# Kernel optimization log

Measured on AMD Instinct MI355X. Metric: run time of the kernel, lower is better.

## Reference

```python
import jax, jax.numpy as jnp
import numpy as np

D = 128          # node_state_dim
N_NODES = 5000
WINDOW = 10
N_TOTAL = WINDOW * N_NODES
E = 131072       # structural (int) edges
T = 2            # message passing steps
HID = 1024


def setup_inputs() -> dict:
    key = jax.random.key(0)
    ks = jax.random.split(key, 20)
    ie = jax.random.randint(ks[0], (E, 3), 0, N_NODES, dtype=jnp.int32)
    int_edges = jnp.stack([ie[:, 0] % WINDOW, ie[:, 1], ie[:, 2]], axis=1)
    nodes = jax.random.randint(ks[1], (N_NODES,), 0, 10, dtype=jnp.int32)

    def init(k, shape, scale=0.05):
        return (jax.random.normal(k, shape, jnp.float32) * scale)

    params = dict(
        embed_table=init(ks[2], (10, D)),
        msg_W1=init(ks[3], (2 * D, HID)), msg_b1=jnp.zeros((HID,), jnp.float32),
        msg_W2=init(ks[4], (HID, D)), msg_b2=jnp.zeros((D,), jnp.float32),
        gru_int_W=init(ks[5], (D, 3 * D)), gru_int_U=init(ks[6], (D, 3 * D)),
        gru_int_b=jnp.zeros((2, 3 * D), jnp.float32),
        gru_temp_W=init(ks[7], (D, 3 * D)), gru_temp_U=init(ks[8], (D, 3 * D)),
        gru_temp_b=jnp.zeros((2, 3 * D), jnp.float32),
        ro_W1=init(ks[9], (D, HID)), ro_b1=jnp.zeros((HID,), jnp.float32),
        ro_W2=init(ks[10], (HID, 512)), ro_b2=jnp.zeros((512,), jnp.float32),
        ro_W3=init(ks[11], (512, 10)), ro_b3=jnp.zeros((10,), jnp.float32),
    )
    return {"int_edges": int_edges, "nodes": nodes, **params}


def _temp_edges():
    fwd_src = np.arange(0, N_TOTAL - N_NODES)
    fwd_dst = fwd_src + N_NODES
    bwd_src = np.arange(N_NODES, N_TOTAL)
    bwd_dst = bwd_src - N_NODES
    src = jnp.asarray(np.concatenate([fwd_src, bwd_src]), jnp.int32)
    dst = jnp.asarray(np.concatenate([fwd_dst, bwd_dst]), jnp.int32)
    return src, dst


def _gru(x, h, W, U, b):
    # Keras GRUCell, reset_after=True. x,h: [N,D]; W,U: [D,3D]; b: [2,3D]
    xg = x @ W + b[0]
    hg = h @ U + b[1]
    xz, xr, xh = jnp.split(xg, 3, axis=-1)
    hz, hr, hh = jnp.split(hg, 3, axis=-1)
    z = jax.nn.sigmoid(xz + hz)
    r = jax.nn.sigmoid(xr + hr)
    hcand = jnp.tanh(xh + r * hh)
    return z * h + (1.0 - z) * hcand


def _msg(x, W1, b1, W2, b2):
    # Dense(1024,relu) -> Dropout(inference: identity) -> Dense(D,relu)
    return jax.nn.relu(jax.nn.relu(x @ W1 + b1) @ W2 + b2)


def _seg_mean(x, idx, n):
    s = jax.ops.segment_sum(x, idx, num_segments=n)
    c = jax.ops.segment_sum(jnp.ones((x.shape[0],), x.dtype), idx, num_segments=n)
    return jnp.where(c[:, None] > 0, s / jnp.maximum(c, 1.0)[:, None], 0.0)


def reference(int_edges, nodes, embed_table, msg_W1, msg_b1, msg_W2, msg_b2,
              gru_int_W, gru_int_U, gru_int_b, gru_temp_W, gru_temp_U, gru_temp_b,
              ro_W1, ro_b1, ro_W2, ro_b2, ro_W3, ro_b3):
    node_idx = int_edges[:, 0] * N_NODES + int_edges[:, 1]        # [E]
    neigh_idx = int_edges[:, 0] * N_NODES + int_edges[:, 2]       # [E]
    t_src, t_dst = _temp_edges()

    h = embed_table[nodes]                                        # [n_nodes, D]
    h = jnp.repeat(h, WINDOW, axis=0)                             # [N_TOTAL, D]

    for _ in range(T):
        # structural edges
        m_in = jnp.concatenate([h[node_idx], h[neigh_idx]], axis=1)   # [E, 2D]
        m = _msg(m_in, msg_W1, msg_b1, msg_W2, msg_b2)                # [E, D]
        agg = _seg_mean(m, neigh_idx, N_TOTAL)                        # [N_TOTAL, D]
        h = _gru(agg, h, gru_int_W, gru_int_U, gru_int_b)
        # temporal edges
        tm_in = jnp.concatenate([h[t_src], h[t_dst]], axis=1)
        tm = _msg(tm_in, msg_W1, msg_b1, msg_W2, msg_b2)
        tagg = _seg_mean(tm, t_dst, N_TOTAL)
        h = _gru(tagg, h, gru_temp_W, gru_temp_U, gru_temp_b)

    # readout on first frame's nodes
    x = h[:N_NODES]
    x = jax.nn.relu(x @ ro_W1 + ro_b1)
    x = jax.nn.relu(x @ ro_W2 + ro_b2)
    return jax.nn.softmax(x @ ro_W3 + ro_b3, axis=-1)
```

## Files before the change

### kernel.cpp

```cpp
#include <hip/hip_runtime.h>
#include <math.h>

#define D 128
#define N_NODES 5000
#define WINDOW 10
#define N_TOTAL 50000
#define NE_INT 131072
#define NE_TMP 90000
#define NE_FWD (N_TOTAL - N_NODES)
#define HID 1024

typedef short bf16x8 __attribute__((ext_vector_type(8)));
typedef float f32x4 __attribute__((ext_vector_type(4)));

#define SA 264
#define SH 136
#define SK 136
#define SCAN_B 256

static __device__ __forceinline__ short f2bf(float f) {
    union { float f; unsigned u; } v; v.f = f;
    unsigned r = v.u + 0x7fffu + ((v.u >> 16) & 1u);
    return (short)(r >> 16);
}
static __device__ __forceinline__ float bf2f(short s) {
    union { unsigned u; float f; } v;
    v.u = ((unsigned)(unsigned short)s) << 16;
    return v.f;
}
static __device__ __forceinline__ float lo_bf(unsigned u) {
    union { unsigned u; float f; } v; v.u = u << 16; return v.f;
}
static __device__ __forceinline__ float hi_bf(unsigned u) {
    union { unsigned u; float f; } v; v.u = u & 0xffff0000u; return v.f;
}

__global__ void k_tcvt(const float* __restrict__ in, short* __restrict__ out, int K, int N) {
    int i = blockIdx.x * blockDim.x + threadIdx.x;
    if (i >= N * K) return;
    int n = i / K, k = i - n * K;
    out[i] = f2bf(in[(size_t)k * N + n]);
}

__global__ void k_init_h(const int* __restrict__ nodes, const float* __restrict__ embed,
                         float* __restrict__ h32, short* __restrict__ h16) {
    int i = blockIdx.x * blockDim.x + threadIdx.x;
    if (i >= N_TOTAL * D) return;
    int row = i >> 7;
    int c = i & 127;
    int n = nodes[row / WINDOW];
    float v = embed[n * D + c];
    h32[i] = v;
    h16[i] = f2bf(v);
}

__global__ void k_build_int_edges(const int* __restrict__ ie, int* __restrict__ src,
                                  int* __restrict__ dst, int* __restrict__ icnt) {
    int e = blockIdx.x * blockDim.x + threadIdx.x;
    if (e >= NE_INT) return;
    int t = ie[e * 3 + 0], a = ie[e * 3 + 1], b = ie[e * 3 + 2];
    int d = t * N_NODES + b;
    src[e] = t * N_NODES + a;
    dst[e] = d;
    atomicAdd(&icnt[d], 1);
}

__global__ void k_build_tmp_edges(int* __restrict__ src, int* __restrict__ dst) {
    int e = blockIdx.x * blockDim.x + threadIdx.x;
    if (e >= NE_TMP) return;
    int s, d;
    if (e < NE_FWD) { s = e; d = e + N_NODES; }
    else { int q = e - NE_FWD; s = q + N_NODES; d = q; }
    src[e] = s;
    dst[e] = d;
}

__global__ void k_scan_partial(const int* __restrict__ cnt, int* __restrict__ rowstart,
                               int* __restrict__ btot, int n) {
    __shared__ int s[SCAN_B];
    int tid = threadIdx.x;
    int i = blockIdx.x * SCAN_B + tid;
    int v = (i < n) ? cnt[i] : 0;
    s[tid] = v;
    __syncthreads();
    for (int off = 1; off < SCAN_B; off <<= 1) {
        int x = (tid >= off) ? s[tid - off] : 0;
        __syncthreads();
        s[tid] += x;
        __syncthreads();
    }
    if (i < n) rowstart[i] = s[tid] - v;
    if (tid == SCAN_B - 1) btot[blockIdx.x] = s[tid];
}

__global__ void k_scan_block(int* __restrict__ btot, int nb) {
    __shared__ int s[SCAN_B];
    int tid = threadIdx.x;
    int v = (tid < nb) ? btot[tid] : 0;
    s[tid] = v;
    __syncthreads();
    for (int off = 1; off < SCAN_B; off <<= 1) {
        int x = (tid >= off) ? s[tid - off] : 0;
        __syncthreads();
        s[tid] += x;
        __syncthreads();
    }
    if (tid < nb) btot[tid] = s[tid] - v;
}

__global__ void k_scan_add(int* __restrict__ rowstart, const int* __restrict__ btot,
                           int* __restrict__ cursor, int n, int total) {
    int i = blockIdx.x * blockDim.x + threadIdx.x;
    if (i < n) {
        int v = rowstart[i] + btot[i >> 8];
        rowstart[i] = v;
        cursor[i] = v;
    }
    if (i == 0) rowstart[n] = total;
}

__global__ void k_fill_csr(const int* __restrict__ dst, int nE, int* __restrict__ cursor,
                           int* __restrict__ pmap) {
    int e = blockIdx.x * blockDim.x + threadIdx.x;
    if (e >= nE) return;
    int p = atomicAdd(&cursor[dst[e]], 1);
    pmap[e] = p;
}

__global__ void __launch_bounds__(256, 2) k_msg_mfma(
    const short* __restrict__ h16, const int* __restrict__ src, const int* __restrict__ dst,
    const int* __restrict__ pmap, int nE,
    const short* __restrict__ W1T, const float* __restrict__ b1,
    const short* __restrict__ W2T, const float* __restrict__ b2,
    short* __restrict__ m)
{
    __shared__ short Ain[64 * SA];
    __shared__ short Hid[64 * SH];

    int t = threadIdx.x;
    int e0 = blockIdx.x * 64;

    {
        int r = t >> 2, q = t & 3;
        int e = e0 + r;
        int ec = (e < nE) ? e : (nE - 1);
        int s = src[ec], d = dst[ec];
        const uint4* ps = (const uint4*)(h16 + (size_t)s * D);
        const uint4* pd = (const uint4*)(h16 + (size_t)d * D);
        uint4* ao = (uint4*)(Ain + r * SA);
#pragma unroll
        for (int i = 0; i < 8; ++i) {
            int g = i * 4 + q;
            ao[g] = (i < 4) ? ps[g] : pd[g - 16];
        }
    }
    __syncthreads();

    int w = t >> 6, lane = t & 63;
    int lm = lane & 15, lk = lane >> 4;

    f32x4 c2[2][4];
#pragma unroll
    for (int cs = 0; cs < 2; ++cs) {
        int out0 = w * 32 + cs * 16 + lk * 4;
#pragma unroll
        for (int et = 0; et < 4; ++et)
#pragma unroll
            for (int rg = 0; rg < 4; ++rg) c2[cs][et][rg] = b2[out0 + rg];
    }

    f32x4 c1[2][4];
#pragma unroll
    for (int cs = 0; cs < 2; ++cs) {
        int ch0 = (2 * w + cs) * 16 + lk * 4;
#pragma unroll
        for (int et = 0; et < 4; ++et)
#pragma unroll
            for (int rg = 0; rg < 4; ++rg) c1[cs][et][rg] = b1[ch0 + rg];
    }
#pragma unroll
    for (int kk = 0; kk < 8; ++kk) {
        int ko = kk * 32 + lk * 8;
        bf16x8 a0 = *(const bf16x8*)(W1T + (size_t)((2 * w) * 16 + lm) * 256 + ko);
        bf16x8 a1 = *(const bf16x8*)(W1T + (size_t)((2 * w + 1) * 16 + lm) * 256 + ko);
        bf16x8 bf[4];
#pragma unroll
        for (int et = 0; et < 4; ++et)
            bf[et] = *(const bf16x8*)(Ain + (et * 16 + lm) * SA + ko);
#pragma unroll
        for (int et = 0; et < 4; ++et) {
            c1[0][et] = __builtin_amdgcn_mfma_f32_16x16x32_bf16(a0, bf[et], c1[0][et], 0, 0, 0);
            c1[1][et] = __builtin_amdgcn_mfma_f32_16x16x32_bf16(a1, bf[et], c1[1][et], 0, 0, 0);
        }
    }

    for (int hc = 0; hc < 8; ++hc) {
        __syncthreads();
#pragma unroll
        for (int cs = 0; cs < 2; ++cs) {
            int ch_in = (2 * w + cs) * 16 + lk * 4;
#pragma unroll
            for (int et = 0; et < 4; ++et) {
                int edge = et * 16 + lm;
                short4 sv;
                sv.x = f2bf(fmaxf(c1[cs][et][0], 0.f));
                sv.y = f2bf(fmaxf(c1[cs][et][1], 0.f));
                sv.z = f2bf(fmaxf(c1[cs][et][2], 0.f));
                sv.w = f2bf(fmaxf(c1[cs][et][3], 0.f));
                *(short4*)(Hid + edge * SH + ch_in) = sv;
            }
        }
        __syncthreads();

        if (hc < 7) {
#pragma unroll
            for (int cs = 0; cs < 2; ++cs) {
                int ch0 = (hc + 1) * 128 + (2 * w + cs) * 16 + lk * 4;
#pragma unroll
                for (int et = 0; et < 4; ++et)
#pragma unroll
                    for (int rg = 0; rg < 4; ++rg) c1[cs][et][rg] = b1[ch0 + rg];
            }
        }
#pragma unroll
        for (int kk = 0; kk < 8; ++kk) {
            int ko = kk * 32 + lk * 8;
            if (kk < 4) {
                bf16x8 a0 = *(const bf16x8*)(W2T + (size_t)(w * 32 + lm) * 1024 + hc * 128 + ko);
                bf16x8 a1 = *(const bf16x8*)(W2T + (size_t)(w * 32 + 16 + lm) * 1024 + hc * 128 + ko);
                bf16x8 bf[4];
#pragma unroll
                for (int et = 0; et < 4; ++et)
                    bf[et] = *(const bf16x8*)(Hid + (et * 16 + lm) * SH + ko);
#pragma unroll
                for (int et = 0; et < 4; ++et) {
                    c2[0][et] = __builtin_amdgcn_mfma_f32_16x16x32_bf16(a0, bf[et], c2[0][et], 0, 0, 0);
                    c2[1][et] = __builtin_amdgcn_mfma_f32_16x16x32_bf16(a1, bf[et], c2[1][et], 0, 0, 0);
                }
            }
            if (hc < 7) {
                bf16x8 a0 = *(const bf16x8*)(W1T + (size_t)((hc + 1) * 128 + (2 * w) * 16 + lm) * 256 + ko);
                bf16x8 a1 = *(const bf16x8*)(W1T + (size_t)((hc + 1) * 128 + (2 * w + 1) * 16 + lm) * 256 + ko);
                bf16x8 bf[4];
#pragma unroll
                for (int et = 0; et < 4; ++et)
                    bf[et] = *(const bf16x8*)(Ain + (et * 16 + lm) * SA + ko);
#pragma unroll
                for (int et = 0; et < 4; ++et) {
                    c1[0][et] = __builtin_amdgcn_mfma_f32_16x16x32_bf16(a0, bf[et], c1[0][et], 0, 0, 0);
                    c1[1][et] = __builtin_amdgcn_mfma_f32_16x16x32_bf16(a1, bf[et], c1[1][et], 0, 0, 0);
                }
            }
        }
    }

#pragma unroll
    for (int et = 0; et < 4; ++et) {
        int edge = et * 16 + lm;
        int e = e0 + edge;
        if (e >= nE) continue;
        int slot = pmap ? pmap[e] : e;
        short* rowp = m + (size_t)slot * 128;
#pragma unroll
        for (int cs = 0; cs < 2; ++cs) {
            int out0 = w * 32 + cs * 16 + lk * 4;
            short4 sv;
            sv.x = f2bf(fmaxf(c2[cs][et][0], 0.f));
            sv.y = f2bf(fmaxf(c2[cs][et][1], 0.f));
            sv.z = f2bf(fmaxf(c2[cs][et][2], 0.f));
            sv.w = f2bf(fmaxf(c2[cs][et][3], 0.f));
            *(short4*)(rowp + out0) = sv;
        }
    }
}

__global__ void __launch_bounds__(256, 2) k_gru_mfma(
    const short* __restrict__ m, const int* __restrict__ rowstart, int mode,
    float* __restrict__ h32, short* __restrict__ h16,
    const short* __restrict__ WT, const short* __restrict__ UT,
    const float* __restrict__ b)
{
    __shared__ short Ax[64 * SK];
    __shared__ short Hx[64 * SK];
    int t = threadIdx.x;
    int r0 = blockIdx.x * 64;

    {
        int r = t >> 2, q = t & 3;
        int row = r0 + r;
        int rc = (row < N_TOTAL) ? row : (N_TOTAL - 1);
        const uint4* hp = (const uint4*)(h16 + (size_t)rc * D);
        uint4* hxo = (uint4*)(Hx + r * SK);
#pragma unroll
        for (int i = 0; i < 4; ++i) hxo[q * 4 + i] = hp[q * 4 + i];

        float acc[32];
#pragma unroll
        for (int i = 0; i < 32; ++i) acc[i] = 0.f;
        int deg = 0;
        if (row < N_TOTAL) {
            if (mode == 0) {
                int s0 = rowstart[row], s1 = rowstart[row + 1];
                deg = s1 - s0;
                for (int p = s0; p < s1; ++p) {
                    const uint4* mp = (const uint4*)(m + (size_t)p * 128 + q * 32);
#pragma unroll
                    for (int i = 0; i < 4; ++i) {
                        uint4 v = mp[i];
                        unsigned ua[4] = {v.x, v.y, v.z, v.w};
#pragma unroll
                        for (int j = 0; j < 4; ++j) {
                            acc[i * 8 + 2 * j]     += lo_bf(ua[j]);
                            acc[i * 8 + 2 * j + 1] += hi_bf(ua[j]);
                        }
                    }
                }
            } else {
                if (row >= N_NODES) {
                    const uint4* mp = (const uint4*)(m + (size_t)(row - N_NODES) * 128 + q * 32);
                    ++deg;
#pragma unroll
                    for (int i = 0; i < 4; ++i) {
                        uint4 v = mp[i];
                        unsigned ua[4] = {v.x, v.y, v.z, v.w};
#pragma unroll
                        for (int j = 0; j < 4; ++j) {
                            acc[i * 8 + 2 * j]     += lo_bf(ua[j]);
                            acc[i * 8 + 2 * j + 1] += hi_bf(ua[j]);
                        }
                    }
                }
                if (row < NE_FWD) {
                    const uint4* mp = (const uint4*)(m + (size_t)(NE_FWD + row) * 128 + q * 32);
                    ++deg;
#pragma unroll
                    for (int i = 0; i < 4; ++i) {
                        uint4 v = mp[i];
                        unsigned ua[4] = {v.x, v.y, v.z, v.w};
#pragma unroll
                        for (int j = 0; j < 4; ++j) {
                            acc[i * 8 + 2 * j]     += lo_bf(ua[j]);
                            acc[i * 8 + 2 * j + 1] += hi_bf(ua[j]);
                        }
                    }
                }
            }
        }
        float inv = (deg > 0) ? 1.f / (float)deg : 0.f;
        uint4* axp = (uint4*)(Ax + r * SK + q * 32);
#pragma unroll
        for (int i = 0; i < 4; ++i) {
            union { uint4 u; short s[8]; } pk;
#pragma unroll
            for (int j = 0; j < 8; ++j) pk.s[j] = f2bf(acc[i * 8 + j] * inv);
            axp[i] = pk.u;
        }
    }
    __syncthreads();

    int w = t >> 6, lane = t & 63;
    int lm = lane & 15, lk = lane >> 4;

    for (int g = 0; g < 8; ++g) {
        int ch = g * 16 + lm;
        f32x4 cxz, cxr, cxh, chz, chr_, chh;
#pragma unroll
        for (int rg = 0; rg < 4; ++rg) {
            cxz[rg] = b[ch];        chz[rg] = b[384 + ch];
            cxr[rg] = b[128 + ch];  chr_[rg] = b[384 + 128 + ch];
            cxh[rg] = b[256 + ch];  chh[rg] = b[384 + 256 + ch];
        }
#pragma unroll
        for (int kk = 0; kk < 4; ++kk) {
            int ko = kk * 32 + lk * 8;
            bf16x8 ax = *(const bf16x8*)(Ax + (w * 16 + lm) * SK + ko);
            bf16x8 hx = *(const bf16x8*)(Hx + (w * 16 + lm) * SK + ko);
            bf16x8 bz = *(const bf16x8*)(WT + (size_t)(ch) * 128 + ko);
            bf16x8 br = *(const bf16x8*)(WT + (size_t)(128 + ch) * 128 + ko);
            bf16x8 bh = *(const bf16x8*)(WT + (size_t)(256 + ch) * 128 + ko);
            bf16x8 uz = *(const bf16x8*)(UT + (size_t)(ch) * 128 + ko);
            bf16x8 ur = *(const bf16x8*)(UT + (size_t)(128 + ch) * 128 + ko);
            bf16x8 uh = *(const bf16x8*)(UT + (size_t)(256 + ch) * 128 + ko);
            cxz = __builtin_amdgcn_mfma_f32_16x16x32_bf16(ax, bz, cxz, 0, 0, 0);
            cxr = __builtin_amdgcn_mfma_f32_16x16x32_bf16(ax, br, cxr, 0, 0, 0);
            cxh = __builtin_amdgcn_mfma_f32_16x16x32_bf16(ax, bh, cxh, 0, 0, 0);
            chz = __builtin_amdgcn_mfma_f32_16x16x32_bf16(hx, uz, chz, 0, 0, 0);
            chr_ = __builtin_amdgcn_mfma_f32_16x16x32_bf16(hx, ur, chr_, 0, 0, 0);
            chh = __builtin_amdgcn_mfma_f32_16x16x32_bf16(hx, uh, chh, 0, 0, 0);
        }
#pragma unroll
        for (int rg = 0; rg < 4; ++rg) {
            int row = r0 + w * 16 + lk * 4 + rg;
            if (row >= N_TOTAL) continue;
            float z = 1.f / (1.f + expf(-(cxz[rg] + chz[rg])));
            float r_ = 1.f / (1.f + expf(-(cxr[rg] + chr_[rg])));
            float hcv = tanhf(cxh[rg] + r_ * chh[rg]);
            size_t idx = (size_t)row * D + ch;
            float hold = h32[idx];
            float hnew = z * hold + (1.f - z) * hcv;
            h32[idx] = hnew;
            h16[idx] = f2bf(hnew);
        }
    }
}

__global__ void __launch_bounds__(256, 2) k_ro_mfma(
    const short* __restrict__ A16, const short* __restrict__ BT,
    const float* __restrict__ bias, float* __restrict__ C32, short* __restrict__ C16,
    int M, int N, int K)
{
    __shared__ short As[64 * SK];
    int t = threadIdx.x;
    int mb = blockIdx.y * 64;
    int nb = blockIdx.x * 128;
    int w = t >> 6, lane = t & 63;
    int lm = lane & 15, lk = lane >> 4;

    f32x4 acc[8];
#pragma unroll
    for (int nt = 0; nt < 8; ++nt) {
        float bv = bias[nb + nt * 16 + lm];
        acc[nt][0] = bv; acc[nt][1] = bv; acc[nt][2] = bv; acc[nt][3] = bv;
    }

    for (int kc = 0; kc < K; kc += 128) {
        __syncthreads();
        {
            int r = t >> 2, q = t & 3;
            int row = mb + r;
            int rc = (row < M) ? row : (M - 1);
            const uint4* ap = (const uint4*)(A16 + (size_t)rc * K + kc);
            uint4* ao = (uint4*)(As + r * SK);
#pragma unroll
            for (int i = 0; i < 4; ++i) ao[i * 4 + q] = ap[i * 4 + q];
        }
        __syncthreads();
#pragma unroll
        for (int kk = 0; kk < 4; ++kk) {
            int ko = kk * 32 + lk * 8;
            bf16x8 a = *(const bf16x8*)(As + (w * 16 + lm) * SK + ko);
#pragma unroll
            for (int nt = 0; nt < 8; ++nt) {
                bf16x8 bfr = *(const bf16x8*)(BT + (size_t)(nb + nt * 16 + lm) * K + kc + ko);
                acc[nt] = __builtin_amdgcn_mfma_f32_16x16x32_bf16(a, bfr, acc[nt], 0, 0, 0);
            }
        }
    }
#pragma unroll
    for (int nt = 0; nt < 8; ++nt) {
        int col = nb + nt * 16 + lm;
#pragma unroll
        for (int rg = 0; rg < 4; ++rg) {
            int row = mb + w * 16 + lk * 4 + rg;
            if (row >= M) continue;
            float v = fmaxf(acc[nt][rg], 0.f);
            if (C32) C32[(size_t)row * N + col] = v;
            if (C16) C16[(size_t)row * N + col] = f2bf(v);
        }
    }
}

__global__ void __launch_bounds__(64) k_logits_softmax(
    const float* __restrict__ r2, const float* __restrict__ W3,
    const float* __restrict__ b3, float* __restrict__ out)
{
    int row = blockIdx.x;
    int t = threadIdx.x;
    float p[10];
#pragma unroll
    for (int j = 0; j < 10; ++j) p[j] = 0.f;
    for (int k = t; k < 512; k += 64) {
        float v = r2[(size_t)row * 512 + k];
#pragma unroll
        for (int j = 0; j < 10; ++j) p[j] += v * W3[k * 10 + j];
    }
#pragma unroll
    for (int j = 0; j < 10; ++j) {
        float s = p[j];
        for (int off = 32; off > 0; off >>= 1) s += __shfl_down(s, off);
        p[j] = s;
    }
    if (t == 0) {
        float mx = -1e30f;
#pragma unroll
        for (int j = 0; j < 10; ++j) { p[j] += b3[j]; mx = fmaxf(mx, p[j]); }
        float sum = 0.f;
#pragma unroll
        for (int j = 0; j < 10; ++j) { p[j] = expf(p[j] - mx); sum += p[j]; }
        float inv = 1.f / sum;
#pragma unroll
        for (int j = 0; j < 10; ++j) out[(size_t)row * 10 + j] = p[j] * inv;
    }
}

extern "C" void kernel_launch(void* const* d_in, const int* in_sizes, int n_in,
                              void* d_out, int out_size, void* d_ws, size_t ws_size,
                              hipStream_t stream)
{
    const int*   ie    = (const int*)d_in[0];
    const int*   nodes = (const int*)d_in[1];
    const float* embed = (const float*)d_in[2];
    const float* mW1   = (const float*)d_in[3];
    const float* mb1   = (const float*)d_in[4];
    const float* mW2   = (const float*)d_in[5];
    const float* mb2   = (const float*)d_in[6];
    const float* giW   = (const float*)d_in[7];
    const float* giU   = (const float*)d_in[8];
    const float* gib   = (const float*)d_in[9];
    const float* gtW   = (const float*)d_in[10];
    const float* gtU   = (const float*)d_in[11];
    const float* gtb   = (const float*)d_in[12];
    const float* rW1   = (const float*)d_in[13];
    const float* rb1   = (const float*)d_in[14];
    const float* rW2   = (const float*)d_in[15];
    const float* rb2   = (const float*)d_in[16];
    const float* rW3   = (const float*)d_in[17];
    const float* rb3   = (const float*)d_in[18];
    float* out = (float*)d_out;

    char* ws = (char*)d_ws;
    size_t off = 0;
    auto alloc = [&](size_t bytes) {
        void* p = ws + off;
        off += (bytes + 255) & ~(size_t)255;
        return p;
    };
    float* h32   = (float*)alloc((size_t)N_TOTAL * D * 4);
    short* h16   = (short*)alloc((size_t)N_TOTAL * D * 2);
    short* m     = (short*)alloc((size_t)NE_INT * 128 * 2);
    int*   icnt  = (int*)alloc((size_t)N_TOTAL * 4);
    int*   rowst = (int*)alloc((size_t)(N_TOTAL + 1) * 4);
    int*   btot  = (int*)alloc(256 * 4);
    int*   curs  = (int*)alloc((size_t)N_TOTAL * 4);
    int*   pmap  = (int*)alloc((size_t)NE_INT * 4);
    int*   srcA  = (int*)alloc((size_t)NE_INT * 4);
    int*   dstA  = (int*)alloc((size_t)NE_INT * 4);
    int*   srcT  = (int*)alloc((size_t)NE_TMP * 4);
    int*   dstT  = (int*)alloc((size_t)NE_TMP * 4);
    short* mW1T  = (short*)alloc((size_t)HID * 256 * 2);
    short* mW2T  = (short*)alloc((size_t)D * HID * 2);
    short* giWT  = (short*)alloc((size_t)384 * D * 2);
    short* giUT  = (short*)alloc((size_t)384 * D * 2);
    short* gtWT  = (short*)alloc((size_t)384 * D * 2);
    short* gtUT  = (short*)alloc((size_t)384 * D * 2);
    short* rW1T  = (short*)alloc((size_t)HID * D * 2);
    short* rW2T  = (short*)alloc((size_t)512 * HID * 2);
    short* r1_16 = (short*)alloc((size_t)N_NODES * HID * 2);
    float* r2_32 = (float*)alloc((size_t)N_NODES * 512 * 4);

    auto tc = [&](const float* in, short* o, int K, int N) {
        k_tcvt<<<(N * K + 255) / 256, 256, 0, stream>>>(in, o, K, N);
    };
    tc(mW1, mW1T, 256, HID);
    tc(mW2, mW2T, HID, D);
    tc(giW, giWT, D, 384);
    tc(giU, giUT, D, 384);
    tc(gtW, gtWT, D, 384);
    tc(gtU, gtUT, D, 384);
    tc(rW1, rW1T, D, HID);
    tc(rW2, rW2T, HID, 512);

    hipMemsetAsync(icnt, 0, (size_t)N_TOTAL * 4, stream);
    k_init_h<<<(N_TOTAL * D + 255) / 256, 256, 0, stream>>>(nodes, embed, h32, h16);
    k_build_int_edges<<<(NE_INT + 255) / 256, 256, 0, stream>>>(ie, srcA, dstA, icnt);
    k_build_tmp_edges<<<(NE_TMP + 255) / 256, 256, 0, stream>>>(srcT, dstT);
    int nb = (N_TOTAL + SCAN_B - 1) / SCAN_B;
    k_scan_partial<<<nb, SCAN_B, 0, stream>>>(icnt, rowst, btot, N_TOTAL);
    k_scan_block<<<1, SCAN_B, 0, stream>>>(btot, nb);
    k_scan_add<<<nb, SCAN_B, 0, stream>>>(rowst, btot, curs, N_TOTAL, NE_INT);
    k_fill_csr<<<(NE_INT + 255) / 256, 256, 0, stream>>>(dstA, NE_INT, curs, pmap);

    int gmsgA = (NE_INT + 63) / 64;
    int gmsgT = (NE_TMP + 63) / 64;
    int ggru = (N_TOTAL + 63) / 64;
    for (int it = 0; it < 2; ++it) {
        k_msg_mfma<<<gmsgA, 256, 0, stream>>>(h16, srcA, dstA, pmap, NE_INT, mW1T, mb1, mW2T, mb2, m);
        k_gru_mfma<<<ggru, 256, 0, stream>>>(m, rowst, 0, h32, h16, giWT, giUT, gib);

        k_msg_mfma<<<gmsgT, 256, 0, stream>>>(h16, srcT, dstT, (const int*)nullptr, NE_TMP, mW1T, mb1, mW2T, mb2, m);
        k_gru_mfma<<<ggru, 256, 0, stream>>>(m, rowst, 1, h32, h16, gtWT, gtUT, gtb);
    }

    dim3 g1(HID / 128, (N_NODES + 63) / 64);
    k_ro_mfma<<<g1, 256, 0, stream>>>(h16, rW1T, rb1, (float*)nullptr, r1_16, N_NODES, HID, D);
    dim3 g2(512 / 128, (N_NODES + 63) / 64);
    k_ro_mfma<<<g2, 256, 0, stream>>>(r1_16, rW2T, rb2, r2_32, (short*)nullptr, N_NODES, 512, HID);
    k_logits_softmax<<<N_NODES, 64, 0, stream>>>(r2_32, rW3, rb3, out);
}
```

Before: 1.298 ms.

## Double edge tile to 128 per block and drop cross-chunk layer-1 prefetch

The message MLP kernel now processes 128 edges per block instead of 64, so each weight fragment loaded from global memory is reused across twice as many edges. The software pipeline that overlapped the next hidden chunk's layer-1 MFMAs with the current layer-2 MFMAs is removed in favour of a simple sequential compute-then-consume loop per chunk. Accumulator registers roughly double and LDS use doubles, so launch bounds drop to one block per SM. This risks lower occupancy and less latency hiding. The gather is also reorganized so each of two threads per edge copies a full source or destination row.

```diff
diff --git a/kernel.cpp b/kernel.cpp
--- a/kernel.cpp
+++ b/kernel.cpp
@@ -127,31 +127,32 @@
     pmap[e] = p;
 }
 
-__global__ void __launch_bounds__(256, 2) k_msg_mfma(
+__global__ void __launch_bounds__(256, 1) k_msg_mfma(
     const short* __restrict__ h16, const int* __restrict__ src, const int* __restrict__ dst,
     const int* __restrict__ pmap, int nE,
     const short* __restrict__ W1T, const float* __restrict__ b1,
     const short* __restrict__ W2T, const float* __restrict__ b2,
     short* __restrict__ m)
 {
-    __shared__ short Ain[64 * SA];
-    __shared__ short Hid[64 * SH];
+    __shared__ short Ain[128 * SA];
+    __shared__ short Hid[128 * SH];
 
     int t = threadIdx.x;
-    int e0 = blockIdx.x * 64;
+    int e0 = blockIdx.x * 128;
 
     {
-        int r = t >> 2, q = t & 3;
+        int r = t >> 1, q = t & 1;
         int e = e0 + r;
         int ec = (e < nE) ? e : (nE - 1);
-        int s = src[ec], d = dst[ec];
-        const uint4* ps = (const uint4*)(h16 + (size_t)s * D);
-        const uint4* pd = (const uint4*)(h16 + (size_t)d * D);
         uint4* ao = (uint4*)(Ain + r * SA);
-#pragma unroll
-        for (int i = 0; i < 8; ++i) {
-            int g = i * 4 + q;
-            ao[g] = (i < 4) ? ps[g] : pd[g - 16];
+        if (q == 0) {
+            const uint4* ps = (const uint4*)(h16 + (size_t)src[ec] * D);
+#pragma unroll
+            for (int i = 0; i < 16; ++i) ao[i] = ps[i];
+        } else {
+            const uint4* pd = (const uint4*)(h16 + (size_t)dst[ec] * D);
+#pragma unroll
+            for (int i = 0; i < 16; ++i) ao[16 + i] = pd[i];
         }
     }
     __syncthreads();
@@ -159,48 +160,47 @@
     int w = t >> 6, lane = t & 63;
     int lm = lane & 15, lk = lane >> 4;
 
-    f32x4 c2[2][4];
+    f32x4 c2[2][8];
 #pragma unroll
     for (int cs = 0; cs < 2; ++cs) {
         int out0 = w * 32 + cs * 16 + lk * 4;
 #pragma unroll
-        for (int et = 0; et < 4; ++et)
+        for (int et = 0; et < 8; ++et)
 #pragma unroll
             for (int rg = 0; rg < 4; ++rg) c2[cs][et][rg] = b2[out0 + rg];
     }
 
-    f32x4 c1[2][4];
-#pragma unroll
-    for (int cs = 0; cs < 2; ++cs) {
-        int ch0 = (2 * w + cs) * 16 + lk * 4;
-#pragma unroll
-        for (int et = 0; et < 4; ++et)
-#pragma unroll
-            for (int rg = 0; rg < 4; ++rg) c1[cs][et][rg] = b1[ch0 + rg];
-    }
-#pragma unroll
-    for (int kk = 0; kk < 8; ++kk) {
-        int ko = kk * 32 + lk * 8;
-        bf16x8 a0 = *(const bf16x8*)(W1T + (size_t)((2 * w) * 16 + lm) * 256 + ko);
-        bf16x8 a1 = *(const bf16x8*)(W1T + (size_t)((2 * w + 1) * 16 + lm) * 256 + ko);
-        bf16x8 bf[4];
-#pragma unroll
-        for (int et = 0; et < 4; ++et)
-            bf[et] = *(const bf16x8*)(Ain + (et * 16 + lm) * SA + ko);
-#pragma unroll
-        for (int et = 0; et < 4; ++et) {
-            c1[0][et] = __builtin_amdgcn_mfma_f32_16x16x32_bf16(a0, bf[et], c1[0][et], 0, 0, 0);
-            c1[1][et] = __builtin_amdgcn_mfma_f32_16x16x32_bf16(a1, bf[et], c1[1][et], 0, 0, 0);
-        }
-    }
-
     for (int hc = 0; hc < 8; ++hc) {
-        __syncthreads();
+        f32x4 c1[2][8];
 #pragma unroll
         for (int cs = 0; cs < 2; ++cs) {
-            int ch_in = (2 * w + cs) * 16 + lk * 4;
-#pragma unroll
-            for (int et = 0; et < 4; ++et) {
+            int ch0 = hc * 128 + w * 32 + cs * 16 + lk * 4;
+#pragma unroll
+            for (int et = 0; et < 8; ++et)
+#pragma unroll
+                for (int rg = 0; rg < 4; ++rg) c1[cs][et][rg] = b1[ch0 + rg];
+        }
+#pragma unroll
+        for (int kk = 0; kk < 8; ++kk) {
+            int ko = kk * 32 + lk * 8;
+            bf16x8 a0 = *(const bf16x8*)(W1T + (size_t)(hc * 128 + w * 32 + lm) * 256 + ko);
+            bf16x8 a1 = *(const bf16x8*)(W1T + (size_t)(hc * 128 + w * 32 + 16 + lm) * 256 + ko);
+            bf16x8 bf[8];
+#pragma unroll
+            for (int et = 0; et < 8; ++et)
+                bf[et] = *(const bf16x8*)(Ain + (et * 16 + lm) * SA + ko);
+#pragma unroll
+            for (int et = 0; et < 8; ++et) {
+                c1[0][et] = __builtin_amdgcn_mfma_f32_16x16x32_bf16(a0, bf[et], c1[0][et], 0, 0, 0);
+                c1[1][et] = __builtin_amdgcn_mfma_f32_16x16x32_bf16(a1, bf[et], c1[1][et], 0, 0, 0);
+            }
+        }
+        __syncthreads();
+#pragma unroll
+        for (int cs = 0; cs < 2; ++cs) {
+            int ch_in = w * 32 + cs * 16 + lk * 4;
+#pragma unroll
+            for (int et = 0; et < 8; ++et) {
                 int edge = et * 16 + lm;
                 short4 sv;
                 sv.x = f2bf(fmaxf(c1[cs][et][0], 0.f));
@@ -212,50 +212,25 @@
         }
         __syncthreads();
 
-        if (hc < 7) {
-#pragma unroll
-            for (int cs = 0; cs < 2; ++cs) {
-                int ch0 = (hc + 1) * 128 + (2 * w + cs) * 16 + lk * 4;
-#pragma unroll
-                for (int et = 0; et < 4; ++et)
-#pragma unroll
-                    for (int rg = 0; rg < 4; ++rg) c1[cs][et][rg] = b1[ch0 + rg];
+#pragma unroll
+        for (int kk = 0; kk < 4; ++kk) {
+            int ko = kk * 32 + lk * 8;
+            bf16x8 a0 = *(const bf16x8*)(W2T + (size_t)(w * 32 + lm) * 1024 + hc * 128 + ko);
+            bf16x8 a1 = *(const bf16x8*)(W2T + (size_t)(w * 32 + 16 + lm) * 1024 + hc * 128 + ko);
+            bf16x8 bf[8];
+#pragma unroll
+            for (int et = 0; et < 8; ++et)
+                bf[et] = *(const bf16x8*)(Hid + (et * 16 + lm) * SH + ko);
+#pragma unroll
+            for (int et = 0; et < 8; ++et) {
+                c2[0][et] = __builtin_amdgcn_mfma_f32_16x16x32_bf16(a0, bf[et], c2[0][et], 0, 0, 0);
+                c2[1][et] = __builtin_amdgcn_mfma_f32_16x16x32_bf16(a1, bf[et], c2[1][et], 0, 0, 0);
             }
         }
-#pragma unroll
-        for (int kk = 0; kk < 8; ++kk) {
-            int ko = kk * 32 + lk * 8;
-            if (kk < 4) {
-                bf16x8 a0 = *(const bf16x8*)(W2T + (size_t)(w * 32 + lm) * 1024 + hc * 128 + ko);
-                bf16x8 a1 = *(const bf16x8*)(W2T + (size_t)(w * 32 + 16 + lm) * 1024 + hc * 128 + ko);
-                bf16x8 bf[4];
-#pragma unroll
-                for (int et = 0; et < 4; ++et)
-                    bf[et] = *(const bf16x8*)(Hid + (et * 16 + lm) * SH + ko);
-#pragma unroll
-                for (int et = 0; et < 4; ++et) {
-                    c2[0][et] = __builtin_amdgcn_mfma_f32_16x16x32_bf16(a0, bf[et], c2[0][et], 0, 0, 0);
-                    c2[1][et] = __builtin_amdgcn_mfma_f32_16x16x32_bf16(a1, bf[et], c2[1][et], 0, 0, 0);
-                }
-            }
-            if (hc < 7) {
-                bf16x8 a0 = *(const bf16x8*)(W1T + (size_t)((hc + 1) * 128 + (2 * w) * 16 + lm) * 256 + ko);
-                bf16x8 a1 = *(const bf16x8*)(W1T + (size_t)((hc + 1) * 128 + (2 * w + 1) * 16 + lm) * 256 + ko);
-                bf16x8 bf[4];
-#pragma unroll
-                for (int et = 0; et < 4; ++et)
-                    bf[et] = *(const bf16x8*)(Ain + (et * 16 + lm) * SA + ko);
-#pragma unroll
-                for (int et = 0; et < 4; ++et) {
-                    c1[0][et] = __builtin_amdgcn_mfma_f32_16x16x32_bf16(a0, bf[et], c1[0][et], 0, 0, 0);
-                    c1[1][et] = __builtin_amdgcn_mfma_f32_16x16x32_bf16(a1, bf[et], c1[1][et], 0, 0, 0);
-                }
-            }
-        }
-    }
-
-#pragma unroll
-    for (int et = 0; et < 4; ++et) {
+    }
+
+#pragma unroll
+    for (int et = 0; et < 8; ++et) {
         int edge = et * 16 + lm;
         int e = e0 + edge;
         if (e >= nE) continue;
@@ -570,8 +545,8 @@
     k_scan_add<<<nb, SCAN_B, 0, stream>>>(rowst, btot, curs, N_TOTAL, NE_INT);
     k_fill_csr<<<(NE_INT + 255) / 256, 256, 0, stream>>>(dstA, NE_INT, curs, pmap);
 
-    int gmsgA = (NE_INT + 63) / 64;
-    int gmsgT = (NE_TMP + 63) / 64;
+    int gmsgA = (NE_INT + 127) / 128;
+    int gmsgT = (NE_TMP + 127) / 128;
     int ggru = (N_TOTAL + 63) / 64;
     for (int it = 0; it < 2; ++it) {
         k_msg_mfma<<<gmsgA, 256, 0, stream>>>(h16, srcA, dstA, pmap, NE_INT, mW1T, mb1, mW2T, mb2, m);
```

Result: faster. 1.256 ms (-3.2%).
